# Performance work log

Measured on AMD Instinct MI355X. Metric: run time of the kernel, lower is better.

## Reference

```python
import jax, jax.numpy as jnp
import numpy as np

N, E, H, DIN, NL = 16384, 524288, 128, 1024, 3
H4 = 4 * H
EPS = 1e-7  # GENConv message eps


def _ln(x, g, b, eps=1e-5):
    mu = jnp.mean(x, axis=-1, keepdims=True)
    var = jnp.var(x, axis=-1, keepdims=True)
    return (x - mu) * jax.lax.rsqrt(var + eps) * g + b


def _genconv(x, src, dst, ew, w1, b1, lng, lnb, w2, b2, t):
    # message: relu(x_j + edge_weight) + eps  -> [E, H]
    msg = jax.nn.relu(x[src] + ew[:, None]) + EPS
    # softmax aggregation with learnable temperature t over incoming edges
    logit = msg * t
    m = jax.ops.segment_max(logit, dst, num_segments=N)
    m = jnp.where(jnp.isfinite(m), m, 0.0)
    e = jnp.exp(logit - m[dst])
    denom = jax.ops.segment_sum(e, dst, num_segments=N)
    alpha = e / (denom[dst] + 1e-16)
    agg = jax.ops.segment_sum(msg * alpha, dst, num_segments=N)  # [N, H]
    h = agg + x  # GENConv adds root features before MLP
    # MLP: Linear(H,2H) -> LayerNorm -> ReLU -> Linear(2H,H)
    return jax.nn.relu(_ln(h @ w1 + b1, lng, lnb)) @ w2 + b2


def _forward(edge_index, features, edge_weight, fc_w, fc_b, conv_w1, conv_b1,
             conv_lng, conv_lnb, conv_w2, conv_b2, conv_t, blk_lng, blk_lnb,
             phi_w, phi_b, attn_wa, attn_ba, attn_wb, attn_bb, attn_wc, attn_bc,
             rho_w, rho_b, clf_w, clf_b):
    src, dst = edge_index[0], edge_index[1]
    x = jax.nn.relu(features @ fc_w + fc_b)  # [N, H]
    x_ = x
    # layers[0]: conv only (no norm/act/residual)
    x = _genconv(x, src, dst, edge_weight, conv_w1[0], conv_b1[0], conv_lng[0],
                 conv_lnb[0], conv_w2[0], conv_b2[0], conv_t[0])
    x_ = jnp.concatenate([x_, x], axis=1)
    # layers[1:]: DeepGCNLayer block='res': x + relu(LN(conv(x))) (eval: dropout=id)
    for i in (1, 2):
        h = _genconv(x, src, dst, edge_weight, conv_w1[i], conv_b1[i], conv_lng[i],
                     conv_lnb[i], conv_w2[i], conv_b2[i], conv_t[i])
        h = jax.nn.relu(_ln(h, blk_lng[i], blk_lnb[i]))
        x = x + h
        x_ = jnp.concatenate([x_, x], axis=1)
    # x_: [N, 4H]
    hp = jax.nn.relu(x_ @ phi_w + phi_b)
    a = jnp.tanh(hp @ attn_wa + attn_ba)
    b = jax.nn.sigmoid(hp @ attn_wb + attn_bb)
    A = (a * b) @ attn_wc + attn_bc  # [N, 1]
    w = jax.nn.softmax(A[:, 0])      # softmax over nodes
    pooled = w @ hp                  # [4H]
    out = jax.nn.relu(pooled @ rho_w + rho_b)
    return out @ clf_w + clf_b       # [num_classes]


def setup_inputs() -> dict:
    key = jax.random.key(0)
    ks = jax.random.split(key, 16)
    sc = 0.05
    rn = lambda k, shp: jax.random.normal(k, shp, jnp.float32) * sc
    return {
        "features": jax.random.normal(ks[0], (N, DIN), jnp.float32),
        "edge_index": jax.random.randint(ks[1], (2, E), 0, N),
        "edge_weight": jax.random.uniform(ks[2], (E,), jnp.float32),
        "fc_w": rn(ks[3], (DIN, H)), "fc_b": jnp.zeros((H,), jnp.float32),
        "conv_w1": rn(ks[4], (NL, H, 2 * H)), "conv_b1": jnp.zeros((NL, 2 * H), jnp.float32),
        "conv_lng": jnp.ones((NL, 2 * H), jnp.float32), "conv_lnb": jnp.zeros((NL, 2 * H), jnp.float32),
        "conv_w2": rn(ks[5], (NL, 2 * H, H)), "conv_b2": jnp.zeros((NL, H), jnp.float32),
        "conv_t": jnp.ones((NL,), jnp.float32),
        "blk_lng": jnp.ones((NL, H), jnp.float32), "blk_lnb": jnp.zeros((NL, H), jnp.float32),
        "phi_w": rn(ks[6], (H4, H4)), "phi_b": jnp.zeros((H4,), jnp.float32),
        "attn_wa": rn(ks[7], (H4, H4)), "attn_ba": jnp.zeros((H4,), jnp.float32),
        "attn_wb": rn(ks[8], (H4, H4)), "attn_bb": jnp.zeros((H4,), jnp.float32),
        "attn_wc": rn(ks[9], (H4, 1)), "attn_bc": jnp.zeros((1,), jnp.float32),
        "rho_w": rn(ks[10], (H4, H4)), "rho_b": jnp.zeros((H4,), jnp.float32),
        "clf_w": rn(ks[11], (H4, 3)), "clf_b": jnp.zeros((3,), jnp.float32),
    }


def reference(features, edge_index, edge_weight, fc_w, fc_b, conv_w1, conv_b1,
              conv_lng, conv_lnb, conv_w2, conv_b2, conv_t, blk_lng, blk_lnb,
              phi_w, phi_b, attn_wa, attn_ba, attn_wb, attn_bb, attn_wc, attn_bc,
              rho_w, rho_b, clf_w, clf_b):
    return _forward(edge_index, features, edge_weight, fc_w, fc_b, conv_w1, conv_b1,
                    conv_lng, conv_lnb, conv_w2, conv_b2, conv_t, blk_lng, blk_lnb,
                    phi_w, phi_b, attn_wa, attn_ba, attn_wb, attn_bb, attn_wc,
                    attn_bc, rho_w, rho_b, clf_w, clf_b)
```

## Files before the change

kernel.cpp:

```cpp
#include <hip/hip_runtime.h>
#include <hip/hip_bf16.h>
#include <cstdint>
#include <cstddef>

#define N_NODES 16384
#define N_EDGES 524288

using bf16 = __hip_bfloat16;
typedef short bf16x8 __attribute__((ext_vector_type(8)));
typedef float f32x4 __attribute__((ext_vector_type(4)));

__device__ __forceinline__ float bf2f(bf16 v) { return __bfloat162float(v); }
__device__ __forceinline__ float ldv(const void* p, size_t i, int f32) {
    return f32 ? ((const float*)p)[i] : bf2f(((const bf16*)p)[i]);
}
__device__ __forceinline__ float us2f(unsigned short u) {
    unsigned int x = ((unsigned int)u) << 16;
    return __uint_as_float(x);
}
__device__ __forceinline__ unsigned short f2us(float f) {
    bf16 b = __float2bfloat16(f);
    return *(unsigned short*)&b;
}
__device__ __forceinline__ float ftanh(float v) { return 1.f - 2.f / (__expf(2.f * v) + 1.f); }
__device__ __forceinline__ float fsig(float v)  { return 1.f / (1.f + __expf(-v)); }

__global__ void zero_k(const unsigned int* __restrict__ lng, int* __restrict__ dtf,
                       uint4* __restrict__ base, int n16) {
    if (blockIdx.x == 0 && threadIdx.x == 0)
        dtf[0] = (lng[0] == 0x3F800000u) ? 1 : 0;
    uint4 z = {0, 0, 0, 0};
    for (int i = blockIdx.x * blockDim.x + threadIdx.x; i < n16; i += gridDim.x * blockDim.x)
        base[i] = z;
}

__global__ void conv_feat_k(const float* __restrict__ in, bf16* __restrict__ out,
                            const int* __restrict__ dtf, int n4) {
    if (!dtf[0]) return;
    for (int i = blockIdx.x * blockDim.x + threadIdx.x; i < n4; i += gridDim.x * blockDim.x) {
        float4 v = ((const float4*)in)[i];
        ushort4 o;
        o.x = f2us(v.x); o.y = f2us(v.y); o.z = f2us(v.z); o.w = f2us(v.w);
        ((ushort4*)out)[i] = o;
    }
}

#define NSEG 10
struct TranspDesc {
    const void* W[NSEG];
    bf16* WT[NSEG];
    int woff[NSEG];
    int lk[NSEG];
    int N[NSEG];
    int ostride[NSEG];
    int start[NSEG + 1];
};

__global__ void transp_all_k(TranspDesc d, const int* __restrict__ dtf, int total) {
    int f32 = dtf[0];
    int i = blockIdx.x * blockDim.x + threadIdx.x;
    if (i >= total) return;
    int s = 0;
    #pragma unroll
    for (int j = 1; j < NSEG; j++) if (i >= d.start[j]) s = j;
    int local = i - d.start[s];
    int lk = d.lk[s];
    int n = local >> lk;
    int k = local & ((1 << lk) - 1);
    d.WT[s][(size_t)n * d.ostride[s] + k] =
        __float2bfloat16(ldv(d.W[s], (size_t)d.woff[s] + (size_t)k * d.N[s] + n, f32));
}

#define GLD(gp, lp) __builtin_amdgcn_global_load_lds( \
    (const __attribute__((address_space(1))) void*)(gp), \
    (__attribute__((address_space(3))) void*)(lp), 16, 0, 0)

template <int ACT, int PIPE, int MR>
__global__ __launch_bounds__(256) void mgemm_k(
    const bf16* __restrict__ A, const bf16* __restrict__ Aalt, int sel, int lda,
    const bf16* __restrict__ WT,
    const void* __restrict__ bias, const void* __restrict__ bias2, size_t boff,
    bf16* __restrict__ C, int ldc, int K, const int* __restrict__ dtf,
    const void* __restrict__ aux1, const void* __restrict__ aux2, size_t aoff,
    const bf16* __restrict__ xold, bf16* __restrict__ xnew,
    float* __restrict__ Aout)
{
    constexpr int NI  = MR / 32;
    constexpr int NP  = MR / 16;
    constexpr int TSZ = MR * 32 + 128 * 32;
    constexpr int LREQ = (PIPE ? 2 * TSZ : TSZ);
    constexpr int LBUF = (MR * 128 > LREQ) ? MR * 128 : LREQ;
    __shared__ unsigned short lbuf[LBUF];
    __shared__ float wcs[64];
    const int f32 = dtf[0];
    const bf16* Ap = (sel && f32) ? Aalt : A;
    int tid = threadIdx.x;
    int wave = tid >> 6, lane = tid & 63;
    int row0 = blockIdx.x * MR, col0 = blockIdx.y * 128;
    const bf16* Ag = Ap + (size_t)row0 * lda;
    const bf16* Bg = WT + (size_t)col0 * K;

    f32x4 acc[NI][4] = {};
    int fr = lane & 15, fg = lane >> 4;
    int wr = (wave >> 1) * (MR / 2), wc = (wave & 1) * 64;
    int rchunk = fg ^ ((fr >> 1) & 3);

    if (ACT == 4 && tid < 64) wcs[tid] = ldv(aux1, (size_t)(col0 >> 1) + tid, f32);

    if constexpr (PIPE == 0) {
        static_assert(MR == 128, "PIPE=0 path hardcodes 128-row geometry");
        unsigned short* lA0 = lbuf;
        unsigned short* lA1 = lbuf + 4096;
        unsigned short* lB0 = lbuf + 8192;
        unsigned short* lB1 = lbuf + 12288;
        for (int k0 = 0; k0 < K; k0 += 64) {
            #pragma unroll
            for (int j = 0; j < 2; j++) {
                int li = j * 256 + tid;
                int r = li >> 2, kc = li & 3;
                int kcs = kc ^ ((r >> 1) & 3);
                char* dA = (char*)lA0 + j * 4096 + wave * 1024;
                char* dB = (char*)lB0 + j * 4096 + wave * 1024;
                GLD(Ag + (size_t)r * lda + k0 + kcs * 8, dA);
                GLD(Bg + (size_t)r * K   + k0 + kcs * 8, dB);
            }
            #pragma unroll
            for (int j = 0; j < 2; j++) {
                int li = j * 256 + tid;
                int r = li >> 2, kc = li & 3;
                int kcs = kc ^ ((r >> 1) & 3);
                char* dA = (char*)lA1 + j * 4096 + wave * 1024;
                char* dB = (char*)lB1 + j * 4096 + wave * 1024;
                GLD(Ag + (size_t)r * lda + k0 + 32 + kcs * 8, dA);
                GLD(Bg + (size_t)r * K   + k0 + 32 + kcs * 8, dB);
            }
            __syncthreads();
            {
                bf16x8 aF[4], bF[4];
                #pragma unroll
                for (int i = 0; i < 4; i++) {
                    aF[i] = *(const bf16x8*)&lA0[(wr + i * 16 + fr) * 32 + rchunk * 8];
                    bF[i] = *(const bf16x8*)&lB0[(wc + i * 16 + fr) * 32 + rchunk * 8];
                }
                #pragma unroll
                for (int i = 0; i < 4; i++)
                    #pragma unroll
                    for (int j = 0; j < 4; j++)
                        acc[i][j] = __builtin_amdgcn_mfma_f32_16x16x32_bf16(aF[i], bF[j], acc[i][j], 0, 0, 0);
            }
            {
                bf16x8 aF[4], bF[4];
                #pragma unroll
                for (int i = 0; i < 4; i++) {
                    aF[i] = *(const bf16x8*)&lA1[(wr + i * 16 + fr) * 32 + rchunk * 8];
                    bF[i] = *(const bf16x8*)&lB1[(wc + i * 16 + fr) * 32 + rchunk * 8];
                }
                #pragma unroll
                for (int i = 0; i < 4; i++)
                    #pragma unroll
                    for (int j = 0; j < 4; j++)
                        acc[i][j] = __builtin_amdgcn_mfma_f32_16x16x32_bf16(aF[i], bF[j], acc[i][j], 0, 0, 0);
            }
            __syncthreads();
        }
    } else {
        auto stage = [&](unsigned short* dst, int k0) {
            #pragma unroll
            for (int j = 0; j < MR / 64; j++) {
                int li = j * 256 + tid;
                int r = li >> 2, kc = li & 3;
                int kcs = kc ^ ((r >> 1) & 3);
                GLD(Ag + (size_t)r * lda + k0 + kcs * 8, (char*)dst + li * 16);
            }
            #pragma unroll
            for (int j = 0; j < 2; j++) {
                int li = j * 256 + tid;
                int r = li >> 2, kc = li & 3;
                int kcs = kc ^ ((r >> 1) & 3);
                GLD(Bg + (size_t)r * K + k0 + kcs * 8, (char*)(dst + MR * 32) + li * 16);
            }
        };
        auto compute = [&](const unsigned short* sA) {
            const unsigned short* sB = sA + MR * 32;
            bf16x8 aF[NI], bF[4];
            #pragma unroll
            for (int i = 0; i < NI; i++)
                aF[i] = *(const bf16x8*)&sA[(wr + i * 16 + fr) * 32 + rchunk * 8];
            #pragma unroll
            for (int j = 0; j < 4; j++)
                bF[j] = *(const bf16x8*)&sB[(wc + j * 16 + fr) * 32 + rchunk * 8];
            #pragma unroll
            for (int i = 0; i < NI; i++)
                #pragma unroll
                for (int j = 0; j < 4; j++)
                    acc[i][j] = __builtin_amdgcn_mfma_f32_16x16x32_bf16(aF[i], bF[j], acc[i][j], 0, 0, 0);
        };

        stage(lbuf, 0);
        int bsel = 0;
        for (int k0 = 0; k0 < K; k0 += 32) {
            __syncthreads();
            if (k0 + 32 < K) stage(lbuf + (bsel ^ 1) * TSZ, k0 + 32);
            compute(lbuf + bsel * TSZ);
            bsel ^= 1;
        }
        __syncthreads();
    }

    unsigned short* lC = lbuf;
    #pragma unroll
    for (int j = 0; j < 4; j++) {
        int col = wc + j * 16 + fr;
        float bv;
        if (ACT == 4) {
            int pair = (col0 + col) >> 1;
            bv = (fr & 1) ? ldv(bias2, pair, f32) : ldv(bias, pair, f32);
        } else {
            bv = ldv(bias, boff + col0 + col, f32);
        }
        #pragma unroll
        for (int i = 0; i < NI; i++) {
            #pragma unroll
            for (int rr = 0; rr < 4; rr++) {
                int row = wr + i * 16 + fg * 4 + rr;
                float v = acc[i][j][rr] + bv;
                if (ACT == 1) v = fmaxf(v, 0.f);
                else if (ACT == 2) v = ftanh(v);
                else if (ACT == 3) v = fsig(v);
                else if (ACT == 4) v = (fr & 1) ? fsig(v) : ftanh(v);
                int scol = col ^ ((row & 3) << 5);
                lC[row * 128 + scol] = f2us(v);
            }
        }
    }
    __syncthreads();

    if (ACT == 4) {
        int p0 = (tid & 15) * 4;
        #pragma unroll
        for (int pass = 0; pass < NP; pass++) {
            int r = pass * 16 + (tid >> 4);
            int sc = ((tid & 15) * 8) ^ ((r & 3) << 5);
            unsigned short v[8];
            *(uint4*)v = *(const uint4*)&lC[r * 128 + sc];
            float s = us2f(v[0]) * us2f(v[1]) * wcs[p0]
                    + us2f(v[2]) * us2f(v[3]) * wcs[p0 + 1]
                    + us2f(v[4]) * us2f(v[5]) * wcs[p0 + 2]
                    + us2f(v[6]) * us2f(v[7]) * wcs[p0 + 3];
            #pragma unroll
            for (int m = 1; m < 16; m <<= 1) s += __shfl_xor(s, m, 64);
            if ((tid & 15) == 0) atomicAdd(&Aout[row0 + r], s);
        }
        return;
    }

    if (ACT == 5) {
        int cl = (tid & 15) * 8;
        float gr[8], brr[8];
        #pragma unroll
        for (int k = 0; k < 8; k++) {
            gr[k]  = ldv(aux1, aoff + cl + k, f32);
            brr[k] = ldv(aux2, aoff + cl + k, f32);
        }
        #pragma unroll
        for (int pass = 0; pass < NP; pass++) {
            int r = pass * 16 + (tid >> 4);
            int sc = cl ^ ((r & 3) << 5);
            unsigned short v[8];
            *(uint4*)v = *(const uint4*)&lC[r * 128 + sc];
            float x[8], s = 0.f;
            #pragma unroll
            for (int k = 0; k < 8; k++) { x[k] = us2f(v[k]); s += x[k]; }
            #pragma unroll
            for (int m = 1; m < 16; m <<= 1) s += __shfl_xor(s, m, 64);
            float mu = s * (1.f / 128.f);
            float q = 0.f;
            #pragma unroll
            for (int k = 0; k < 8; k++) { x[k] -= mu; q += x[k] * x[k]; }
            #pragma unroll
            for (int m = 1; m < 16; m <<= 1) q += __shfl_xor(q, m, 64);
            float rstd = rsqrtf(q * (1.f / 128.f) + 1e-5f);
            unsigned short xo[8], o[8];
            *(uint4*)xo = *(const uint4*)(xold + (size_t)(row0 + r) * 512 + cl);
            #pragma unroll
            for (int k = 0; k < 8; k++) {
                float y = fmaxf(x[k] * rstd * gr[k] + brr[k], 0.f);
                o[k] = f2us(us2f(xo[k]) + y);
            }
            *(uint4*)(xnew + (size_t)(row0 + r) * 512 + cl) = *(const uint4*)o;
        }
        return;
    }

    #pragma unroll
    for (int pass = 0; pass < NP; pass++) {
        int r = pass * 16 + (tid >> 4);
        int c = (tid & 15) * 8;
        int sc = c ^ ((r & 3) << 5);
        *(uint4*)(C + (size_t)(row0 + r) * ldc + col0 + c) = *(const uint4*)&lC[r * 128 + sc];
    }
}

static void* const force_inst_mgemm_ab = (void*)mgemm_k<4, 0, 128>;

__global__ __launch_bounds__(256) void abgemm_k(
    const bf16* __restrict__ A, int lda,
    const bf16* __restrict__ WT,
    const void* __restrict__ bias, const void* __restrict__ bias2,
    int K, const int* __restrict__ dtf,
    const void* __restrict__ aux1,
    float* __restrict__ Aout)
{
    __shared__ unsigned short lbuf[128 * 128];
    __shared__ float wcs[64];
    const int f32 = dtf[0];
    int tid = threadIdx.x;
    int wave = tid >> 6, lane = tid & 63;
    int row0 = blockIdx.x * 128, col0 = blockIdx.y * 128;
    const bf16* Ag = A + (size_t)row0 * lda;
    const bf16* Bg = WT + (size_t)col0 * K;

    f32x4 acc[4][4] = {};
    int fr = lane & 15, fg = lane >> 4;
    int wr = (wave >> 1) * 64, wc = (wave & 1) * 64;
    int rchunk = fg ^ ((fr >> 1) & 3);

    if (tid < 64) wcs[tid] = ldv(aux1, (size_t)(col0 >> 1) + tid, f32);

    unsigned short* lA0 = lbuf;
    unsigned short* lA1 = lbuf + 4096;
    unsigned short* lB0 = lbuf + 8192;
    unsigned short* lB1 = lbuf + 12288;
    for (int k0 = 0; k0 < K; k0 += 64) {
        #pragma unroll
        for (int j = 0; j < 2; j++) {
            int li = j * 256 + tid;
            int r = li >> 2, kc = li & 3;
            int kcs = kc ^ ((r >> 1) & 3);
            char* dA = (char*)lA0 + j * 4096 + wave * 1024;
            char* dB = (char*)lB0 + j * 4096 + wave * 1024;
            GLD(Ag + (size_t)r * lda + k0 + kcs * 8, dA);
            GLD(Bg + (size_t)r * K   + k0 + kcs * 8, dB);
        }
        #pragma unroll
        for (int j = 0; j < 2; j++) {
            int li = j * 256 + tid;
            int r = li >> 2, kc = li & 3;
            int kcs = kc ^ ((r >> 1) & 3);
            char* dA = (char*)lA1 + j * 4096 + wave * 1024;
            char* dB = (char*)lB1 + j * 4096 + wave * 1024;
            GLD(Ag + (size_t)r * lda + k0 + 32 + kcs * 8, dA);
            GLD(Bg + (size_t)r * K   + k0 + 32 + kcs * 8, dB);
        }
        __syncthreads();
        {
            bf16x8 aF[4], bF[4];
            #pragma unroll
            for (int i = 0; i < 4; i++) {
                aF[i] = *(const bf16x8*)&lA0[(wr + i * 16 + fr) * 32 + rchunk * 8];
                bF[i] = *(const bf16x8*)&lB0[(wc + i * 16 + fr) * 32 + rchunk * 8];
            }
            #pragma unroll
            for (int i = 0; i < 4; i++)
                #pragma unroll
                for (int j = 0; j < 4; j++)
                    acc[i][j] = __builtin_amdgcn_mfma_f32_16x16x32_bf16(aF[i], bF[j], acc[i][j], 0, 0, 0);
        }
        {
            bf16x8 aF[4], bF[4];
            #pragma unroll
            for (int i = 0; i < 4; i++) {
                aF[i] = *(const bf16x8*)&lA1[(wr + i * 16 + fr) * 32 + rchunk * 8];
                bF[i] = *(const bf16x8*)&lB1[(wc + i * 16 + fr) * 32 + rchunk * 8];
            }
            #pragma unroll
            for (int i = 0; i < 4; i++)
                #pragma unroll
                for (int j = 0; j < 4; j++)
                    acc[i][j] = __builtin_amdgcn_mfma_f32_16x16x32_bf16(aF[i], bF[j], acc[i][j], 0, 0, 0);
        }
        __syncthreads();
    }

    unsigned short* lC = lbuf;
    #pragma unroll
    for (int j = 0; j < 4; j++) {
        int col = wc + j * 16 + fr;
        int pair = (col0 + col) >> 1;
        float bv = (fr & 1) ? ldv(bias2, pair, f32) : ldv(bias, pair, f32);
        #pragma unroll
        for (int i = 0; i < 4; i++) {
            #pragma unroll
            for (int rr = 0; rr < 4; rr++) {
                int row = wr + i * 16 + fg * 4 + rr;
                float v = acc[i][j][rr] + bv;
                v = (fr & 1) ? fsig(v) : ftanh(v);
                int scol = col ^ ((row & 3) << 5);
                lC[row * 128 + scol] = f2us(v);
            }
        }
    }
    __syncthreads();

    int p0 = (tid & 15) * 4;
    #pragma unroll
    for (int pass = 0; pass < 8; pass++) {
        int r = pass * 16 + (tid >> 4);
        int sc = ((tid & 15) * 8) ^ ((r & 3) << 5);
        unsigned short v[8];
        *(uint4*)v = *(const uint4*)&lC[r * 128 + sc];
        float s = us2f(v[0]) * us2f(v[1]) * wcs[p0]
                + us2f(v[2]) * us2f(v[3]) * wcs[p0 + 1]
                + us2f(v[4]) * us2f(v[5]) * wcs[p0 + 2]
                + us2f(v[6]) * us2f(v[7]) * wcs[p0 + 3];
        #pragma unroll
        for (int m = 1; m < 16; m <<= 1) s += __shfl_xor(s, m, 64);
        if ((tid & 15) == 0) atomicAdd(&Aout[row0 + r], s);
    }
}

__global__ __launch_bounds__(256) void fcgemm_k(
    const float* __restrict__ Af, const bf16* __restrict__ Ab,
    const bf16* __restrict__ WT,
    const void* __restrict__ bias,
    bf16* __restrict__ C, int ldc, const int* __restrict__ dtf)
{
    constexpr int K = 1024;
    constexpr int TSZ = 64 * 32 + 128 * 32;
    __shared__ unsigned short lbuf[2 * TSZ];
    const int f32 = dtf[0];
    int tid = threadIdx.x;
    int wave = tid >> 6, lane = tid & 63;
    int fr = lane & 15, fg = lane >> 4;
    int wr = (wave >> 1) * 32, wc = (wave & 1) * 64;
    int rchunk = fg ^ ((fr >> 1) & 3);
    int row0 = blockIdx.x * 64;
    const float* Agf = Af + (size_t)row0 * K;
    const bf16*  Agb = Ab + (size_t)row0 * K;
    const bf16* Bg = WT;

    f32x4 acc[2][4] = {};

    auto stage = [&](unsigned short* dst, int k0) {
        {
            int r = tid >> 2, kc = tid & 3;
            int kcs = kc ^ ((r >> 1) & 3);
            if (f32) {
                const float* src = Agf + (size_t)r * K + k0 + kcs * 8;
                float4 v0 = *(const float4*)src;
                float4 v1 = *(const float4*)(src + 4);
                unsigned short o[8];
                o[0] = f2us(v0.x); o[1] = f2us(v0.y); o[2] = f2us(v0.z); o[3] = f2us(v0.w);
                o[4] = f2us(v1.x); o[5] = f2us(v1.y); o[6] = f2us(v1.z); o[7] = f2us(v1.w);
                *(uint4*)((char*)dst + tid * 16) = *(const uint4*)o;
            } else {
                GLD(Agb + (size_t)r * K + k0 + kcs * 8, (char*)dst + tid * 16);
            }
        }
        #pragma unroll
        for (int j = 0; j < 2; j++) {
            int li = j * 256 + tid;
            int r = li >> 2, kc = li & 3;
            int kcs = kc ^ ((r >> 1) & 3);
            GLD(Bg + (size_t)r * K + k0 + kcs * 8, (char*)(dst + 64 * 32) + li * 16);
        }
    };

    stage(lbuf, 0);
    int bsel = 0;
    for (int k0 = 0; k0 < K; k0 += 32) {
        __syncthreads();
        if (k0 + 32 < K) stage(lbuf + (bsel ^ 1) * TSZ, k0 + 32);
        const unsigned short* sA = lbuf + bsel * TSZ;
        const unsigned short* sB = sA + 64 * 32;
        bf16x8 aF[2], bF[4];
        #pragma unroll
        for (int i = 0; i < 2; i++)
            aF[i] = *(const bf16x8*)&sA[(wr + i * 16 + fr) * 32 + rchunk * 8];
        #pragma unroll
        for (int j = 0; j < 4; j++)
            bF[j] = *(const bf16x8*)&sB[(wc + j * 16 + fr) * 32 + rchunk * 8];
        #pragma unroll
        for (int i = 0; i < 2; i++)
            #pragma unroll
            for (int j = 0; j < 4; j++)
                acc[i][j] = __builtin_amdgcn_mfma_f32_16x16x32_bf16(aF[i], bF[j], acc[i][j], 0, 0, 0);
        bsel ^= 1;
    }
    __syncthreads();

    unsigned short* lC = lbuf;
    #pragma unroll
    for (int j = 0; j < 4; j++) {
        int col = wc + j * 16 + fr;
        float bv = ldv(bias, col, f32);
        #pragma unroll
        for (int i = 0; i < 2; i++) {
            #pragma unroll
            for (int rr = 0; rr < 4; rr++) {
                int row = wr + i * 16 + fg * 4 + rr;
                float v = fmaxf(acc[i][j][rr] + bv, 0.f);
                int scol = col ^ ((row & 3) << 5);
                lC[row * 128 + scol] = f2us(v);
            }
        }
    }
    __syncthreads();
    #pragma unroll
    for (int pass = 0; pass < 4; pass++) {
        int r = pass * 16 + (tid >> 4);
        int c = (tid & 15) * 8;
        int sc = c ^ ((r & 3) << 5);
        *(uint4*)(C + (size_t)(row0 + r) * ldc + c) = *(const uint4*)&lC[r * 128 + sc];
    }
}

__global__ __launch_bounds__(256) void c1ln_k(
    const bf16* __restrict__ A, const bf16* __restrict__ WT,
    const void* __restrict__ bias, size_t boff,
    const void* __restrict__ g, const void* __restrict__ b, size_t goff,
    const int* __restrict__ dtf, bf16* __restrict__ out)
{
    constexpr int K = 128;
    constexpr int TSZ = 64 * 32 + 256 * 32;
    __shared__ unsigned short lbuf[2 * TSZ];
    const int f32 = dtf[0];
    int tid = threadIdx.x;
    int wave = tid >> 6, lane = tid & 63;
    int fr = lane & 15, fg = lane >> 4;
    int rchunk = fg ^ ((fr >> 1) & 3);
    int row0 = blockIdx.x * 64;
    const bf16* Ag = A + (size_t)row0 * K;
    const bf16* Bg = WT;

    f32x4 acc[16] = {};

    auto stage = [&](unsigned short* dst, int k0) {
        {
            int r = tid >> 2, kc = tid & 3;
            int kcs = kc ^ ((r >> 1) & 3);
            GLD(Ag + (size_t)r * K + k0 + kcs * 8, (char*)dst + tid * 16);
        }
        #pragma unroll
        for (int j = 0; j < 4; j++) {
            int li = j * 256 + tid;
            int r = li >> 2, kc = li & 3;
            int kcs = kc ^ ((r >> 1) & 3);
            GLD(Bg + (size_t)r * K + k0 + kcs * 8, (char*)(dst + 64 * 32) + li * 16);
        }
    };

    stage(lbuf, 0);
    int bsel = 0;
    for (int k0 = 0; k0 < K; k0 += 32) {
        __syncthreads();
        if (k0 + 32 < K) stage(lbuf + (bsel ^ 1) * TSZ, k0 + 32);
        const unsigned short* sA = lbuf + bsel * TSZ;
        const unsigned short* sB = sA + 64 * 32;
        bf16x8 aF = *(const bf16x8*)&sA[(wave * 16 + fr) * 32 + rchunk * 8];
        #pragma unroll
        for (int j = 0; j < 16; j++) {
            bf16x8 bF = *(const bf16x8*)&sB[(j * 16 + fr) * 32 + rchunk * 8];
            acc[j] = __builtin_amdgcn_mfma_f32_16x16x32_bf16(aF, bF, acc[j], 0, 0, 0);
        }
        bsel ^= 1;
    }
    __syncthreads();

    float bv[16], gv[16], bb[16];
    #pragma unroll
    for (int j = 0; j < 16; j++) {
        int col = j * 16 + fr;
        bv[j] = ldv(bias, boff + col, f32);
        gv[j] = ldv(g, goff + col, f32);
        bb[j] = ldv(b, goff + col, f32);
    }
    unsigned short* lC = lbuf;
    #pragma unroll
    for (int rr = 0; rr < 4; rr++) {
        int row = wave * 16 + fg * 4 + rr;
        float v[16], s = 0.f;
        #pragma unroll
        for (int j = 0; j < 16; j++) { v[j] = acc[j][rr] + bv[j]; s += v[j]; }
        #pragma unroll
        for (int m = 1; m < 16; m <<= 1) s += __shfl_xor(s, m, 64);
        float mu = s * (1.f / 256.f);
        float q = 0.f;
        #pragma unroll
        for (int j = 0; j < 16; j++) { v[j] -= mu; q += v[j] * v[j]; }
        #pragma unroll
        for (int m = 1; m < 16; m <<= 1) q += __shfl_xor(q, m, 64);
        float rstd = rsqrtf(q * (1.f / 256.f) + 1e-5f);
        int swz = ((row >> 2) & 3) << 4;
        #pragma unroll
        for (int j = 0; j < 16; j++) {
            int col = j * 16 + fr;
            float y = fmaxf(v[j] * rstd * gv[j] + bb[j], 0.f);
            lC[row * 256 + (col ^ swz)] = f2us(y);
        }
    }
    __syncthreads();
    #pragma unroll
    for (int pass = 0; pass < 8; pass++) {
        int r = pass * 8 + (tid >> 5);
        int c = (tid & 31) * 8;
        int sc = c ^ (((r >> 2) & 3) << 4);
        *(uint4*)(out + (size_t)(row0 + r) * 256 + c) = *(const uint4*)&lC[r * 256 + sc];
    }
}

__global__ void hist_k(const int* __restrict__ dst, int* __restrict__ deg, int E) {
    int e = blockIdx.x * blockDim.x + threadIdx.x;
    if (e < E) atomicAdd(&deg[dst[e]], 1);
}

__global__ __launch_bounds__(1024) void scan_k(const int* __restrict__ deg,
                                               int* __restrict__ offs,
                                               int* __restrict__ cursor, int n) {
    __shared__ int part[1024];
    int tid = threadIdx.x;
    int base = tid * 16;
    int local[16];
    int s = 0;
    #pragma unroll
    for (int i = 0; i < 16; i++) { local[i] = deg[base + i]; s += local[i]; }
    part[tid] = s;
    __syncthreads();
    for (int o = 1; o < 1024; o <<= 1) {
        int v = (tid >= o) ? part[tid - o] : 0;
        __syncthreads();
        part[tid] += v;
        __syncthreads();
    }
    int run = part[tid] - s;
    #pragma unroll
    for (int i = 0; i < 16; i++) {
        offs[base + i] = run;
        cursor[base + i] = run;
        run += local[i];
    }
    if (tid == 1023) offs[n] = run;
}

__global__ void scatter_k(const int* __restrict__ src, const int* __restrict__ dst,
                          const void* __restrict__ ew, const int* __restrict__ dtf,
                          int* __restrict__ cursor, int2* __restrict__ csr_pack, int E) {
    int e = blockIdx.x * blockDim.x + threadIdx.x;
    if (e < E) {
        int f32 = dtf[0];
        int d = dst[e];
        int p = atomicAdd(&cursor[d], 1);
        int2 rec;
        rec.x = src[e];
        rec.y = __float_as_int(ldv(ew, e, f32));
        csr_pack[p] = rec;
    }
}

__global__ __launch_bounds__(256) void agg_k(
    const bf16* __restrict__ xin, int ldx,
    const int* __restrict__ offs, const int2* __restrict__ csr_pack,
    const void* __restrict__ conv_t, int layer, const int* __restrict__ dtf,
    bf16* __restrict__ hout)
{
    __shared__ float red[4][32][9];
    int node = blockIdx.x;
    int tid = threadIdx.x;
    int wv = tid >> 6, lane = tid & 63;
    int hl = lane >> 5, ll = lane & 31;
    int f32 = dtf[0];
    float t = ldv(conv_t, layer, f32);
    int s0 = offs[node], s1 = offs[node + 1];
    float ss0 = 0.f, ss1 = 0.f, ss2 = 0.f, ss3 = 0.f;
    float ws0 = 0.f, ws1 = 0.f, ws2 = 0.f, ws3 = 0.f;
    const bf16* xcol = xin + ll * 4;

    auto body = [&](uint2 xv, float ewv) {
        float x0 = us2f((unsigned short)xv.x);
        float x1 = us2f((unsigned short)(xv.x >> 16));
        float x2 = us2f((unsigned short)xv.y);
        float x3 = us2f((unsigned short)(xv.y >> 16));
        float m0 = fmaxf(x0 + ewv, 0.f) + 1e-7f;
        float m1 = fmaxf(x1 + ewv, 0.f) + 1e-7f;
        float m2 = fmaxf(x2 + ewv, 0.f) + 1e-7f;
        float m3 = fmaxf(x3 + ewv, 0.f) + 1e-7f;
        float e0 = __expf(fminf(m0 * t, 80.f));
        float e1 = __expf(fminf(m1 * t, 80.f));
        float e2 = __expf(fminf(m2 * t, 80.f));
        float e3 = __expf(fminf(m3 * t, 80.f));
        ss0 += e0; ws0 += m0 * e0;
        ss1 += e1; ws1 += m1 * e1;
        ss2 += e2; ws2 += m2 * e2;
        ss3 += e3; ws3 += m3 * e3;
    };

    int p = s0 + wv * 2 + hl;
    for (; p + 8 < s1; p += 16) {
        int2 rA = csr_pack[p];
        int2 rB = csr_pack[p + 8];
        uint2 xa = *(const uint2*)(xcol + (size_t)rA.x * ldx);
        uint2 xb = *(const uint2*)(xcol + (size_t)rB.x * ldx);
        body(xa, __int_as_float(rA.y));
        body(xb, __int_as_float(rB.y));
    }
    if (p < s1) {
        int2 rA = csr_pack[p];
        uint2 xa = *(const uint2*)(xcol + (size_t)rA.x * ldx);
        body(xa, __int_as_float(rA.y));
    }

    ss0 += __shfl_xor(ss0, 32, 64); ws0 += __shfl_xor(ws0, 32, 64);
    ss1 += __shfl_xor(ss1, 32, 64); ws1 += __shfl_xor(ws1, 32, 64);
    ss2 += __shfl_xor(ss2, 32, 64); ws2 += __shfl_xor(ws2, 32, 64);
    ss3 += __shfl_xor(ss3, 32, 64); ws3 += __shfl_xor(ws3, 32, 64);
    if (hl == 0) {
        red[wv][ll][0] = ss0; red[wv][ll][1] = ss1;
        red[wv][ll][2] = ss2; red[wv][ll][3] = ss3;
        red[wv][ll][4] = ws0; red[wv][ll][5] = ws1;
        red[wv][ll][6] = ws2; red[wv][ll][7] = ws3;
    }
    __syncthreads();
    if (tid < 32) {
        float S0 = 0, S1 = 0, S2 = 0, S3 = 0, W0 = 0, W1 = 0, W2 = 0, W3 = 0;
        #pragma unroll
        for (int w = 0; w < 4; w++) {
            S0 += red[w][tid][0]; S1 += red[w][tid][1];
            S2 += red[w][tid][2]; S3 += red[w][tid][3];
            W0 += red[w][tid][4]; W1 += red[w][tid][5];
            W2 += red[w][tid][6]; W3 += red[w][tid][7];
        }
        uint2 sv = *(const uint2*)(xin + (size_t)node * ldx + tid * 4);
        float o0 = W0 / (S0 + 1e-16f) + us2f((unsigned short)sv.x);
        float o1 = W1 / (S1 + 1e-16f) + us2f((unsigned short)(sv.x >> 16));
        float o2 = W2 / (S2 + 1e-16f) + us2f((unsigned short)sv.y);
        float o3 = W3 / (S3 + 1e-16f) + us2f((unsigned short)(sv.y >> 16));
        uint2 ov;
        ov.x = (unsigned int)f2us(o0) | ((unsigned int)f2us(o1) << 16);
        ov.y = (unsigned int)f2us(o2) | ((unsigned int)f2us(o3) << 16);
        *(uint2*)(hout + (size_t)node * 128 + tid * 4) = ov;
    }
}

__global__ __launch_bounds__(256) void pooled_k(const float* __restrict__ A,
                                                const bf16* __restrict__ hp,
                                                float* __restrict__ pooled,
                                                float* __restrict__ sumexp,
                                                int rowsPerBlk) {
    int tid = threadIdx.x;
    int r0 = blockIdx.x * rowsPerBlk;
    float a0 = 0.f, a1 = 0.f, se = 0.f;
    for (int r = 0; r < rowsPerBlk; r++) {
        int n = r0 + r;
        float wn = __expf(A[n]);
        se += wn;
        const bf16* hr = hp + (size_t)n * 512;
        a0 += wn * bf2f(hr[tid]);
        a1 += wn * bf2f(hr[tid + 256]);
    }
    atomicAdd(&pooled[tid], a0);
    atomicAdd(&pooled[tid + 256], a1);
    if (tid == 0) atomicAdd(sumexp, se);
}

__global__ __launch_bounds__(256) void rho_part_k(
    const float* __restrict__ pooled,
    const void* __restrict__ rw,
    const int* __restrict__ dtf,
    float* __restrict__ vacc) {
    int col = blockIdx.x * 256 + threadIdx.x;
    int k0 = blockIdx.y * 16;
    int f32 = dtf[0];
    float acc = 0.f;
    #pragma unroll
    for (int i = 0; i < 16; i++)
        acc = fmaf(pooled[k0 + i], ldv(rw, (size_t)(k0 + i) * 512 + col, f32), acc);
    atomicAdd(&vacc[col], acc);
}

__global__ __launch_bounds__(64) void clf_k(const float* __restrict__ vacc,
                                            const float* __restrict__ sumexp,
                                            const void* __restrict__ rb,
                                            const void* __restrict__ cw,
                                            const void* __restrict__ cb,
                                            const int* __restrict__ dtf,
                                            void* __restrict__ out) {
    int lane = threadIdx.x;
    int f32 = dtf[0];
    float inv = 1.f / (*sumexp);
    #pragma unroll
    for (int t = 0; t < 3; t++) {
        float acc = 0.f;
        for (int j = lane; j < 512; j += 64) {
            float vj = fmaxf(vacc[j] * inv + ldv(rb, j, f32), 0.f);
            acc += vj * ldv(cw, (size_t)j * 3 + t, f32);
        }
        for (int s = 32; s > 0; s >>= 1) acc += __shfl_xor(acc, s, 64);
        if (lane == 0) {
            float o = acc + ldv(cb, t, f32);
            if (f32) ((float*)out)[t] = o;
            else     ((bf16*)out)[t] = __float2bfloat16(o);
        }
    }
}

extern "C" void kernel_launch(void* const* d_in, const int* in_sizes, int n_in,
                              void* d_out, int out_size, void* d_ws, size_t ws_size,
                              hipStream_t stream) {
    const void* features = d_in[0];
    const int*  eidx     = (const int*)d_in[1];
    const void* ew       = d_in[2];
    const void* fc_w     = d_in[3];
    const void* fc_b     = d_in[4];
    const void* conv_w1  = d_in[5];
    const void* conv_b1  = d_in[6];
    const void* conv_lng = d_in[7];
    const void* conv_lnb = d_in[8];
    const void* conv_w2  = d_in[9];
    const void* conv_b2  = d_in[10];
    const void* conv_t   = d_in[11];
    const void* blk_lng  = d_in[12];
    const void* blk_lnb  = d_in[13];
    const void* phi_w    = d_in[14];
    const void* phi_b    = d_in[15];
    const void* attn_wa  = d_in[16];
    const void* attn_ba  = d_in[17];
    const void* attn_wb  = d_in[18];
    const void* attn_bb  = d_in[19];
    const void* attn_wc  = d_in[20];
    const void* rho_w    = d_in[22];
    const void* rho_b    = d_in[23];
    const void* clf_w    = d_in[24];
    const void* clf_b    = d_in[25];

    const int* src = eidx;
    const int* dst = eidx + N_EDGES;

    char* wsp = (char*)d_ws;
    size_t off = 0;
    auto alloc = [&](size_t bytes) -> void* {
        void* p = wsp + off;
        off = (off + bytes + 255) & ~(size_t)255;
        return p;
    };
    int*   dtf    = (int*)alloc(256);
    float* sumexp = (float*)alloc(256);
    float* vec    = (float*)alloc(512 * 4);
    float* pooled = (float*)alloc(512 * 4);
    int*   deg    = (int*)alloc((size_t)N_NODES * 4);
    int*   offs   = (int*)alloc((size_t)(N_NODES + 1) * 4);
    int*   cursor = (int*)alloc((size_t)N_NODES * 4);
    float* Aw     = (float*)alloc((size_t)N_NODES * 4);
    int2*  csr_pack = (int2*)alloc((size_t)N_EDGES * 8);
    bf16* WT_fc  = (bf16*)alloc((size_t)128 * 1024 * 2);
    bf16* WT_c1  = (bf16*)alloc((size_t)3 * 256 * 128 * 2);
    bf16* WT_c2  = (bf16*)alloc((size_t)3 * 128 * 256 * 2);
    bf16* WT_phi = (bf16*)alloc((size_t)512 * 512 * 2);
    bf16* WT_ab  = (bf16*)alloc((size_t)1024 * 512 * 2);
    bf16* x_cat   = (bf16*)alloc((size_t)N_NODES * 512 * 2);
    bf16* scratch = (bf16*)alloc((size_t)N_NODES * 512 * 2);
    bf16* hp      = (bf16*)alloc((size_t)N_NODES * 512 * 2);
    bf16* feat_bf = (bf16*)alloc((size_t)N_NODES * 1024 * 2);

    bf16* h_tmp  = scratch;
    bf16* mid    = scratch + (size_t)N_NODES * 128;

    size_t zbytes = (size_t)((char*)(Aw + N_NODES) - (char*)sumexp);
    zero_k<<<64, 256, 0, stream>>>((const unsigned int*)conv_lng, dtf,
                                   (uint4*)sumexp, (int)(zbytes / 16));

    TranspDesc td{};
    int pos = 0, si = 0;
    auto seg = [&](const void* W, int woff, bf16* WT, int lk, int N, int ostride, int count) {
        td.W[si] = W; td.woff[si] = woff; td.WT[si] = WT;
        td.lk[si] = lk; td.N[si] = N; td.ostride[si] = ostride; td.start[si] = pos;
        pos += count; si++;
    };
    seg(fc_w, 0, WT_fc, 10, 128, 1024, 128 * 1024);
    for (int l = 0; l < 3; l++) seg(conv_w1, l * 128 * 256, WT_c1 + (size_t)l * 256 * 128, 7, 256, 128, 256 * 128);
    for (int l = 0; l < 3; l++) seg(conv_w2, l * 256 * 128, WT_c2 + (size_t)l * 128 * 256, 8, 128, 256, 128 * 256);
    seg(phi_w, 0, WT_phi, 9, 512, 512, 512 * 512);
    seg(attn_wa, 0, WT_ab, 9, 512, 1024, 512 * 512);
    seg(attn_wb, 0, WT_ab + 512, 9, 512, 1024, 512 * 512);
    td.start[NSEG] = pos;
    transp_all_k<<<(pos + 255) / 256, 256, 0, stream>>>(td, dtf, pos);

    hist_k<<<N_EDGES / 256, 256, 0, stream>>>(dst, deg, N_EDGES);
    scan_k<<<1, 1024, 0, stream>>>(deg, offs, cursor, N_NODES);
    scatter_k<<<N_EDGES / 256, 256, 0, stream>>>(src, dst, ew, dtf, cursor, csr_pack, N_EDGES);

    fcgemm_k<<<256, 256, 0, stream>>>(
        (const float*)features, (const bf16*)features, WT_fc, fc_b,
        x_cat, 512, dtf);

    for (int l = 0; l < 3; l++) {
        const bf16* x_in = x_cat + (size_t)l * 128;
        agg_k<<<N_NODES, 256, 0, stream>>>(x_in, 512, offs, csr_pack, conv_t, l, dtf, h_tmp);
        c1ln_k<<<256, 256, 0, stream>>>(
            h_tmp, WT_c1 + (size_t)l * 256 * 128,
            conv_b1, (size_t)l * 256, conv_lng, conv_lnb, (size_t)l * 256,
            dtf, mid);
        if (l == 0) {
            mgemm_k<0, 1, 64><<<dim3(256, 1), 256, 0, stream>>>(
                mid, mid, 0, 256, WT_c2 + (size_t)l * 128 * 256,
                conv_b2, conv_b2, (size_t)l * 128, x_cat + 128, 512, 256, dtf,
                nullptr, nullptr, 0, nullptr, nullptr, nullptr);
        } else {
            mgemm_k<5, 1, 64><<<dim3(256, 1), 256, 0, stream>>>(
                mid, mid, 0, 256, WT_c2 + (size_t)l * 128 * 256,
                conv_b2, conv_b2, (size_t)l * 128, hp , 512, 256, dtf,
                blk_lng, blk_lnb, (size_t)l * 128,
                x_cat + (size_t)l * 128, x_cat + (size_t)(l + 1) * 128, nullptr);
        }
    }

    mgemm_k<1, 1, 64><<<dim3(256, 4), 256, 0, stream>>>(
        x_cat, x_cat, 0, 512, WT_phi, phi_b, phi_b, 0, hp, 512, 512, dtf,
        nullptr, nullptr, 0, nullptr, nullptr, nullptr);
    abgemm_k<<<dim3(128, 8), 256, 0, stream>>>(
        hp, 512, WT_ab, attn_ba, attn_bb, 512, dtf, attn_wc, Aw);
    pooled_k<<<256, 256, 0, stream>>>(Aw, hp, pooled, sumexp, N_NODES / 256);
    rho_part_k<<<dim3(2, 32), 256, 0, stream>>>(pooled, rho_w, dtf, vec);
    clf_k<<<1, 64, 0, stream>>>(vec, sumexp, rho_b, clf_w, clf_b, dtf, d_out);
}
```

Baseline: 485.8 us.

## Tile weight transpose through LDS and deepen attention GEMM K-step to 128

The weight transpose kernel now moves 32x32 tiles through padded shared memory, one block per tile, so both the global reads and the global writes are coalesced. Before, each thread did its own strided scattered access. The attention a/b GEMM loads four 32-wide K slices per barrier pair instead of two. This halves the number of synchronisations but doubles LDS use per block, which may cut occupancy. The unused feature-conversion kernel and its buffer are removed.

```diff
diff --git a/kernel.cpp b/kernel.cpp
--- a/kernel.cpp
+++ b/kernel.cpp
@@ -34,41 +34,43 @@
         base[i] = z;
 }
 
-__global__ void conv_feat_k(const float* __restrict__ in, bf16* __restrict__ out,
-                            const int* __restrict__ dtf, int n4) {
-    if (!dtf[0]) return;
-    for (int i = blockIdx.x * blockDim.x + threadIdx.x; i < n4; i += gridDim.x * blockDim.x) {
-        float4 v = ((const float4*)in)[i];
-        ushort4 o;
-        o.x = f2us(v.x); o.y = f2us(v.y); o.z = f2us(v.z); o.w = f2us(v.w);
-        ((ushort4*)out)[i] = o;
-    }
-}
-
 #define NSEG 10
 struct TranspDesc {
     const void* W[NSEG];
     bf16* WT[NSEG];
     int woff[NSEG];
-    int lk[NSEG];
     int N[NSEG];
     int ostride[NSEG];
-    int start[NSEG + 1];
+    int tstart[NSEG + 1];
 };
 
-__global__ void transp_all_k(TranspDesc d, const int* __restrict__ dtf, int total) {
+__global__ __launch_bounds__(256) void transp_all_k(TranspDesc d, const int* __restrict__ dtf) {
+    __shared__ float tile[32][33];
     int f32 = dtf[0];
-    int i = blockIdx.x * blockDim.x + threadIdx.x;
-    if (i >= total) return;
+    int b = blockIdx.x;
     int s = 0;
     #pragma unroll
-    for (int j = 1; j < NSEG; j++) if (i >= d.start[j]) s = j;
-    int local = i - d.start[s];
-    int lk = d.lk[s];
-    int n = local >> lk;
-    int k = local & ((1 << lk) - 1);
-    d.WT[s][(size_t)n * d.ostride[s] + k] =
-        __float2bfloat16(ldv(d.W[s], (size_t)d.woff[s] + (size_t)k * d.N[s] + n, f32));
+    for (int j = 1; j < NSEG; j++) if (b >= d.tstart[j]) s = j;
+    int tloc = b - d.tstart[s];
+    int N = d.N[s];
+    int tpn = N >> 5;
+    int tk = tloc / tpn, tn = tloc - tk * tpn;
+    int k0 = tk * 32, n0 = tn * 32;
+    int t = threadIdx.x;
+    int c = t & 31, r0 = t >> 5;
+    #pragma unroll
+    for (int j = 0; j < 4; j++) {
+        int r = r0 + 8 * j;
+        tile[r][c] = ldv(d.W[s], (size_t)d.woff[s] + (size_t)(k0 + r) * N + n0 + c, f32);
+    }
+    __syncthreads();
+    bf16* wt = d.WT[s];
+    int ost = d.ostride[s];
+    #pragma unroll
+    for (int j = 0; j < 4; j++) {
+        int r = r0 + 8 * j;
+        wt[(size_t)(n0 + r) * ost + k0 + c] = __float2bfloat16(tile[c][r]);
+    }
 }
 
 #define GLD(gp, lp) __builtin_amdgcn_global_load_lds( \
@@ -311,7 +313,7 @@
     const void* __restrict__ aux1,
     float* __restrict__ Aout)
 {
-    __shared__ unsigned short lbuf[128 * 128];
+    __shared__ unsigned short lbuf[2 * 128 * 128];
     __shared__ float wcs[64];
     const int f32 = dtf[0];
     int tid = threadIdx.x;
@@ -327,51 +329,30 @@
 
     if (tid < 64) wcs[tid] = ldv(aux1, (size_t)(col0 >> 1) + tid, f32);
 
-    unsigned short* lA0 = lbuf;
-    unsigned short* lA1 = lbuf + 4096;
-    unsigned short* lB0 = lbuf + 8192;
-    unsigned short* lB1 = lbuf + 12288;
-    for (int k0 = 0; k0 < K; k0 += 64) {
-        #pragma unroll
-        for (int j = 0; j < 2; j++) {
-            int li = j * 256 + tid;
-            int r = li >> 2, kc = li & 3;
-            int kcs = kc ^ ((r >> 1) & 3);
-            char* dA = (char*)lA0 + j * 4096 + wave * 1024;
-            char* dB = (char*)lB0 + j * 4096 + wave * 1024;
-            GLD(Ag + (size_t)r * lda + k0 + kcs * 8, dA);
-            GLD(Bg + (size_t)r * K   + k0 + kcs * 8, dB);
-        }
-        #pragma unroll
-        for (int j = 0; j < 2; j++) {
-            int li = j * 256 + tid;
-            int r = li >> 2, kc = li & 3;
-            int kcs = kc ^ ((r >> 1) & 3);
-            char* dA = (char*)lA1 + j * 4096 + wave * 1024;
-            char* dB = (char*)lB1 + j * 4096 + wave * 1024;
-            GLD(Ag + (size_t)r * lda + k0 + 32 + kcs * 8, dA);
-            GLD(Bg + (size_t)r * K   + k0 + 32 + kcs * 8, dB);
+    for (int k0 = 0; k0 < K; k0 += 128) {
+        #pragma unroll
+        for (int q = 0; q < 4; q++) {
+            #pragma unroll
+            for (int j = 0; j < 2; j++) {
+                int li = j * 256 + tid;
+                int r = li >> 2, kc = li & 3;
+                int kcs = kc ^ ((r >> 1) & 3);
+                char* dA = (char*)(lbuf + q * 4096) + j * 4096 + wave * 1024;
+                char* dB = (char*)(lbuf + 16384 + q * 4096) + j * 4096 + wave * 1024;
+                GLD(Ag + (size_t)r * lda + k0 + q * 32 + kcs * 8, dA);
+                GLD(Bg + (size_t)r * K   + k0 + q * 32 + kcs * 8, dB);
+            }
         }
         __syncthreads();
-        {
+        #pragma unroll
+        for (int q = 0; q < 4; q++) {
+            const unsigned short* sA = lbuf + q * 4096;
+            const unsigned short* sB = lbuf + 16384 + q * 4096;
             bf16x8 aF[4], bF[4];
             #pragma unroll
             for (int i = 0; i < 4; i++) {
-                aF[i] = *(const bf16x8*)&lA0[(wr + i * 16 + fr) * 32 + rchunk * 8];
-                bF[i] = *(const bf16x8*)&lB0[(wc + i * 16 + fr) * 32 + rchunk * 8];
-            }
-            #pragma unroll
-            for (int i = 0; i < 4; i++)
-                #pragma unroll
-                for (int j = 0; j < 4; j++)
-                    acc[i][j] = __builtin_amdgcn_mfma_f32_16x16x32_bf16(aF[i], bF[j], acc[i][j], 0, 0, 0);
-        }
-        {
-            bf16x8 aF[4], bF[4];
-            #pragma unroll
-            for (int i = 0; i < 4; i++) {
-                aF[i] = *(const bf16x8*)&lA1[(wr + i * 16 + fr) * 32 + rchunk * 8];
-                bF[i] = *(const bf16x8*)&lB1[(wc + i * 16 + fr) * 32 + rchunk * 8];
+                aF[i] = *(const bf16x8*)&sA[(wr + i * 16 + fr) * 32 + rchunk * 8];
+                bF[i] = *(const bf16x8*)&sB[(wc + i * 16 + fr) * 32 + rchunk * 8];
             }
             #pragma unroll
             for (int i = 0; i < 4; i++)
@@ -859,7 +840,6 @@
     bf16* x_cat   = (bf16*)alloc((size_t)N_NODES * 512 * 2);
     bf16* scratch = (bf16*)alloc((size_t)N_NODES * 512 * 2);
     bf16* hp      = (bf16*)alloc((size_t)N_NODES * 512 * 2);
-    bf16* feat_bf = (bf16*)alloc((size_t)N_NODES * 1024 * 2);
 
     bf16* h_tmp  = scratch;
     bf16* mid    = scratch + (size_t)N_NODES * 128;
@@ -870,19 +850,19 @@
 
     TranspDesc td{};
     int pos = 0, si = 0;
-    auto seg = [&](const void* W, int woff, bf16* WT, int lk, int N, int ostride, int count) {
+    auto seg = [&](const void* W, int woff, bf16* WT, int K, int N, int ostride) {
         td.W[si] = W; td.woff[si] = woff; td.WT[si] = WT;
-        td.lk[si] = lk; td.N[si] = N; td.ostride[si] = ostride; td.start[si] = pos;
-        pos += count; si++;
+        td.N[si] = N; td.ostride[si] = ostride; td.tstart[si] = pos;
+        pos += (K / 32) * (N / 32); si++;
     };
-    seg(fc_w, 0, WT_fc, 10, 128, 1024, 128 * 1024);
-    for (int l = 0; l < 3; l++) seg(conv_w1, l * 128 * 256, WT_c1 + (size_t)l * 256 * 128, 7, 256, 128, 256 * 128);
-    for (int l = 0; l < 3; l++) seg(conv_w2, l * 256 * 128, WT_c2 + (size_t)l * 128 * 256, 8, 128, 256, 128 * 256);
-    seg(phi_w, 0, WT_phi, 9, 512, 512, 512 * 512);
-    seg(attn_wa, 0, WT_ab, 9, 512, 1024, 512 * 512);
-    seg(attn_wb, 0, WT_ab + 512, 9, 512, 1024, 512 * 512);
-    td.start[NSEG] = pos;
-    transp_all_k<<<(pos + 255) / 256, 256, 0, stream>>>(td, dtf, pos);
+    seg(fc_w, 0, WT_fc, 1024, 128, 1024);
+    for (int l = 0; l < 3; l++) seg(conv_w1, l * 128 * 256, WT_c1 + (size_t)l * 256 * 128, 128, 256, 128);
+    for (int l = 0; l < 3; l++) seg(conv_w2, l * 256 * 128, WT_c2 + (size_t)l * 128 * 256, 256, 128, 256);
+    seg(phi_w, 0, WT_phi, 512, 512, 512);
+    seg(attn_wa, 0, WT_ab, 512, 512, 1024);
+    seg(attn_wb, 0, WT_ab + 512, 512, 512, 1024);
+    td.tstart[NSEG] = pos;
+    transp_all_k<<<pos, 256, 0, stream>>>(td, dtf);
 
     hist_k<<<N_EDGES / 256, 256, 0, stream>>>(dst, deg, N_EDGES);
     scan_k<<<1, 1024, 0, stream>>>(deg, offs, cursor, N_NODES);
```

Result: no change. 481.9 us (-0.8%).
